# Kernel optimization log

Hardware: AMD Instinct MI355X
Metric: run time of the kernel (lower is better)

The kernel has to match this reference:

```python
import jax, jax.numpy as jnp
import numpy as np

DIM = 1024
RANK = 16


def setup_inputs() -> dict:
    key = jax.random.key(0)
    ks = jax.random.split(key, 9)
    s = 0.02
    return {
        "x": jax.random.normal(ks[0], (2, 4096, DIM), dtype=jnp.float32),
        "W_qkv": jax.random.normal(ks[1], (3 * DIM, DIM), dtype=jnp.float32) * s,
        "b_qkv": jax.random.normal(ks[2], (3 * DIM,), dtype=jnp.float32) * s,
        "A_q": jax.random.normal(ks[3], (RANK, DIM), dtype=jnp.float32) * s,
        "B_q": jax.random.normal(ks[4], (DIM, RANK), dtype=jnp.float32) * s,
        "A_k": jax.random.normal(ks[5], (RANK, DIM), dtype=jnp.float32) * s,
        "B_k": jax.random.normal(ks[6], (DIM, RANK), dtype=jnp.float32) * s,
        "A_v": jax.random.normal(ks[7], (RANK, DIM), dtype=jnp.float32) * s,
        "B_v": jax.random.normal(ks[8], (DIM, RANK), dtype=jnp.float32) * s,
        "alpha": jnp.float32(0.5),
    }


def reference(x, W_qkv, b_qkv, A_q, B_q, A_k, B_k, A_v, B_v, alpha):
    # base fused QKV projection: [B, S, 3*dim]
    qkv = jnp.einsum("bsd,od->bso", x, W_qkv) + b_qkv
    # low-rank adapters: x @ A.T @ B.T, rank=16
    lora_q = jnp.einsum("bsr,dr->bsd", jnp.einsum("bsd,rd->bsr", x, A_q), B_q)
    lora_k = jnp.einsum("bsr,dr->bsd", jnp.einsum("bsd,rd->bsr", x, A_k), B_k)
    lora_v = jnp.einsum("bsr,dr->bsd", jnp.einsum("bsd,rd->bsr", x, A_v), B_v)
    # scaled add into q/k/v slices (concat order matches torch slice layout)
    delta = jnp.concatenate([lora_q, lora_k, lora_v], axis=-1)
    return qkv + alpha * delta
```

## Files before the change

### kernel.cpp

```cpp
#include <hip/hip_runtime.h>
#include <stdint.h>

#define DIM    1024
#define RANK   16
#define M_TOT  8192
#define N_TOT  3072
#define K_TOT  1024

#define BM 128
#define BN 128
#define BK 64

typedef __attribute__((ext_vector_type(8))) short  s8v;
typedef __attribute__((ext_vector_type(4))) float  f4v;

__device__ __forceinline__ unsigned short f2bf(float f) {
    union { float f; unsigned int u; } v; v.f = f;
    unsigned int u = v.u;
    u += 0x7FFFu + ((u >> 16) & 1u);
    return (unsigned short)(u >> 16);
}

__global__ void cvt_x(const float4* __restrict__ x, ushort4* __restrict__ xb, int n4) {
    int i = blockIdx.x * blockDim.x + threadIdx.x;
    if (i < n4) {
        float4 v = x[i];
        ushort4 o;
        o.x = f2bf(v.x); o.y = f2bf(v.y); o.z = f2bf(v.z); o.w = f2bf(v.w);
        xb[i] = o;
    }
}

__global__ void fold_w(const float* __restrict__ W,
                       const float* __restrict__ Aq, const float* __restrict__ Bq,
                       const float* __restrict__ Ak, const float* __restrict__ Bk,
                       const float* __restrict__ Av, const float* __restrict__ Bv,
                       const float* __restrict__ alpha_p,
                       unsigned short* __restrict__ Wb) {
    const int o   = blockIdx.x;
    const int tid = threadIdx.x;
    const int sel  = o >> 10;
    const int orow = o & 1023;
    const float* Am = (sel == 0) ? Aq : (sel == 1) ? Ak : Av;
    const float* Bm = (sel == 0) ? Bq : (sel == 1) ? Bk : Bv;

    __shared__ float sb[RANK];
    if (tid < RANK) sb[tid] = alpha_p[0] * Bm[orow * RANK + tid];
    __syncthreads();

    for (int d = tid; d < DIM; d += 256) {
        float acc = W[o * DIM + d];
        #pragma unroll
        for (int r = 0; r < RANK; ++r)
            acc += sb[r] * Am[r * DIM + d];
        Wb[o * DIM + d] = f2bf(acc);
    }
}

__global__ __launch_bounds__(256, 2)
void gemm_bt(const unsigned short* __restrict__ Xb,
             const unsigned short* __restrict__ Wb,
             const float* __restrict__ bias,
             float* __restrict__ out) {
    __shared__ __align__(16) unsigned short As[BM * BK];
    __shared__ __align__(16) unsigned short Bs[BN * BK];

    const int tid  = threadIdx.x;
    const int wave = tid >> 6;
    const int lane = tid & 63;
    const int l15  = lane & 15;
    const int lq   = lane >> 4;
    const int wr   = wave >> 1;
    const int wc   = wave & 1;

    const int bm = blockIdx.x;
    const int bn = blockIdx.y;

    const unsigned short* aptr[4];
    const unsigned short* bptr[4];
    #pragma unroll
    for (int u = 0; u < 4; ++u) {
        const int c   = wave * 4 + u;
        const int row = ((c >> 1) << 4) + l15;
        const int col = ((c & 1) << 5) + (lq << 3);
        aptr[u] = Xb + (size_t)(bm * BM + row) * K_TOT + col;
        bptr[u] = Wb + (size_t)(bn * BN + row) * K_TOT + col;
    }

    f4v acc[4][4] = {};

    for (int kk = 0; kk < K_TOT; kk += BK) {
        __syncthreads();
        #pragma unroll
        for (int u = 0; u < 4; ++u) {
            const int c = wave * 4 + u;
            __builtin_amdgcn_global_load_lds(
                (const __attribute__((address_space(1))) void*)(aptr[u]),
                (__attribute__((address_space(3))) void*)(&As[c * 512]),
                16, 0, 0);
            __builtin_amdgcn_global_load_lds(
                (const __attribute__((address_space(1))) void*)(bptr[u]),
                (__attribute__((address_space(3))) void*)(&Bs[c * 512]),
                16, 0, 0);
            aptr[u] += BK;
            bptr[u] += BK;
        }
        __syncthreads();

        const s8v* Av = (const s8v*)As;
        const s8v* Bv = (const s8v*)Bs;
        #pragma unroll
        for (int t = 0; t < 2; ++t) {
            s8v af[4], bf[4];
            #pragma unroll
            for (int i = 0; i < 4; ++i) {
                const int ia = wr * 4 + i;
                const int jb = wc * 4 + i;
                af[i] = Av[(ia * 2 + t) * 64 + lane];
                bf[i] = Bv[(jb * 2 + t) * 64 + lane];
            }
            #pragma unroll
            for (int i = 0; i < 4; ++i)
                #pragma unroll
                for (int j = 0; j < 4; ++j)
                    acc[i][j] = __builtin_amdgcn_mfma_f32_16x16x32_bf16(
                        af[i], bf[j], acc[i][j], 0, 0, 0);
        }
    }

    const int col_base = bn * BN + wc * 64;
    const int row_base = bm * BM + wr * 64 + lq * 4;
    #pragma unroll
    for (int j = 0; j < 4; ++j) {
        const int col = col_base + j * 16 + l15;
        const float bv = bias[col];
        #pragma unroll
        for (int i = 0; i < 4; ++i) {
            const int row = row_base + i * 16;
            #pragma unroll
            for (int r = 0; r < 4; ++r)
                out[(size_t)(row + r) * N_TOT + col] = acc[i][j][r] + bv;
        }
    }
}

extern "C" void kernel_launch(void* const* d_in, const int* in_sizes, int n_in,
                              void* d_out, int out_size, void* d_ws, size_t ws_size,
                              hipStream_t stream) {
    const float* x     = (const float*)d_in[0];
    const float* W     = (const float*)d_in[1];
    const float* b     = (const float*)d_in[2];
    const float* Aq    = (const float*)d_in[3];
    const float* Bq    = (const float*)d_in[4];
    const float* Ak    = (const float*)d_in[5];
    const float* Bk    = (const float*)d_in[6];
    const float* Av    = (const float*)d_in[7];
    const float* Bv    = (const float*)d_in[8];
    const float* alpha = (const float*)d_in[9];
    float* out = (float*)d_out;

    unsigned short* xb = (unsigned short*)d_ws;
    unsigned short* Wb = (unsigned short*)((char*)d_ws + (size_t)M_TOT * K_TOT * 2);

    const int n4 = (M_TOT * K_TOT) / 4;
    cvt_x<<<n4 / 256, 256, 0, stream>>>((const float4*)x, (ushort4*)xb, n4);
    fold_w<<<N_TOT, 256, 0, stream>>>(W, Aq, Bq, Ak, Bk, Av, Bv, alpha, Wb);

    dim3 grid(M_TOT / BM, N_TOT / BN);
    gemm_bt<<<grid, 256, 0, stream>>>(xb, Wb, b, out);
}
```

Baseline: 249.9 us.

## Merge prep kernels and shrink GEMM M-tile to 64 for higher occupancy

Folds the x-to-bf16 conversion and the LoRA weight folding into one prep launch, removing a kernel launch gap. The GEMM block tile drops from 128x128 to 64x128. Each wave now computes a 64x32 strip with a 4x2 accumulator array, and launch bounds are raised to 5 blocks per CU. This doubles the grid and raises occupancy to hide latency, at the cost of less data reuse per block and more global traffic for the W tile.

Result: slower. 286.8 us (+14.8%).

```diff
diff --git a/kernel.cpp b/kernel.cpp
--- a/kernel.cpp
+++ b/kernel.cpp
@@ -7,7 +7,7 @@
 #define N_TOT  3072
 #define K_TOT  1024
 
-#define BM 128
+#define BM 64
 #define BN 128
 #define BK 64
 
@@ -21,43 +21,42 @@
     return (unsigned short)(u >> 16);
 }
 
-__global__ void cvt_x(const float4* __restrict__ x, ushort4* __restrict__ xb, int n4) {
-    int i = blockIdx.x * blockDim.x + threadIdx.x;
-    if (i < n4) {
+__global__ void prep(const float4* __restrict__ x, ushort4* __restrict__ xb,
+                     const float* __restrict__ W,
+                     const float* __restrict__ Aq, const float* __restrict__ Bq,
+                     const float* __restrict__ Ak, const float* __restrict__ Bk,
+                     const float* __restrict__ Av, const float* __restrict__ Bv,
+                     const float* __restrict__ alpha_p,
+                     unsigned short* __restrict__ Wb) {
+    const int tid = threadIdx.x;
+    if (blockIdx.x < 8192) {
+        int i = blockIdx.x * 256 + tid;
         float4 v = x[i];
         ushort4 o;
         o.x = f2bf(v.x); o.y = f2bf(v.y); o.z = f2bf(v.z); o.w = f2bf(v.w);
         xb[i] = o;
+    } else {
+        const int o    = blockIdx.x - 8192;
+        const int sel  = o >> 10;
+        const int orow = o & 1023;
+        const float* Am = (sel == 0) ? Aq : (sel == 1) ? Ak : Av;
+        const float* Bm = (sel == 0) ? Bq : (sel == 1) ? Bk : Bv;
+
+        __shared__ float sb[RANK];
+        if (tid < RANK) sb[tid] = alpha_p[0] * Bm[orow * RANK + tid];
+        __syncthreads();
+
+        for (int d = tid; d < DIM; d += 256) {
+            float acc = W[o * DIM + d];
+            #pragma unroll
+            for (int r = 0; r < RANK; ++r)
+                acc += sb[r] * Am[r * DIM + d];
+            Wb[o * DIM + d] = f2bf(acc);
+        }
     }
 }
 
-__global__ void fold_w(const float* __restrict__ W,
-                       const float* __restrict__ Aq, const float* __restrict__ Bq,
-                       const float* __restrict__ Ak, const float* __restrict__ Bk,
-                       const float* __restrict__ Av, const float* __restrict__ Bv,
-                       const float* __restrict__ alpha_p,
-                       unsigned short* __restrict__ Wb) {
-    const int o   = blockIdx.x;
-    const int tid = threadIdx.x;
-    const int sel  = o >> 10;
-    const int orow = o & 1023;
-    const float* Am = (sel == 0) ? Aq : (sel == 1) ? Ak : Av;
-    const float* Bm = (sel == 0) ? Bq : (sel == 1) ? Bk : Bv;
-
-    __shared__ float sb[RANK];
-    if (tid < RANK) sb[tid] = alpha_p[0] * Bm[orow * RANK + tid];
-    __syncthreads();
-
-    for (int d = tid; d < DIM; d += 256) {
-        float acc = W[o * DIM + d];
-        #pragma unroll
-        for (int r = 0; r < RANK; ++r)
-            acc += sb[r] * Am[r * DIM + d];
-        Wb[o * DIM + d] = f2bf(acc);
-    }
-}
-
-__global__ __launch_bounds__(256, 2)
+__global__ __launch_bounds__(256, 5)
 void gemm_bt(const unsigned short* __restrict__ Xb,
              const unsigned short* __restrict__ Wb,
              const float* __restrict__ bias,
@@ -70,76 +69,71 @@
     const int lane = tid & 63;
     const int l15  = lane & 15;
     const int lq   = lane >> 4;
-    const int wr   = wave >> 1;
-    const int wc   = wave & 1;
 
     const int bm = blockIdx.x;
     const int bn = blockIdx.y;
 
-    const unsigned short* aptr[4];
-    const unsigned short* bptr[4];
+    const unsigned short* gptr[6];
+    unsigned short* lptr[6];
     #pragma unroll
-    for (int u = 0; u < 4; ++u) {
-        const int c   = wave * 4 + u;
+    for (int u = 0; u < 6; ++u) {
+        const int q = wave * 6 + u;
+        const int c   = (q < 8) ? q : (q - 8);
         const int row = ((c >> 1) << 4) + l15;
         const int col = ((c & 1) << 5) + (lq << 3);
-        aptr[u] = Xb + (size_t)(bm * BM + row) * K_TOT + col;
-        bptr[u] = Wb + (size_t)(bn * BN + row) * K_TOT + col;
+        if (q < 8) {
+            gptr[u] = Xb + (size_t)(bm * BM + row) * K_TOT + col;
+            lptr[u] = &As[c * 512];
+        } else {
+            gptr[u] = Wb + (size_t)(bn * BN + row) * K_TOT + col;
+            lptr[u] = &Bs[c * 512];
+        }
     }
 
-    f4v acc[4][4] = {};
+    f4v acc[4][2] = {};
 
     for (int kk = 0; kk < K_TOT; kk += BK) {
         __syncthreads();
         #pragma unroll
-        for (int u = 0; u < 4; ++u) {
-            const int c = wave * 4 + u;
+        for (int u = 0; u < 6; ++u) {
             __builtin_amdgcn_global_load_lds(
-                (const __attribute__((address_space(1))) void*)(aptr[u]),
-                (__attribute__((address_space(3))) void*)(&As[c * 512]),
+                (const __attribute__((address_space(1))) void*)(gptr[u]),
+                (__attribute__((address_space(3))) void*)(lptr[u]),
                 16, 0, 0);
-            __builtin_amdgcn_global_load_lds(
-                (const __attribute__((address_space(1))) void*)(bptr[u]),
-                (__attribute__((address_space(3))) void*)(&Bs[c * 512]),
-                16, 0, 0);
-            aptr[u] += BK;
-            bptr[u] += BK;
+            gptr[u] += BK;
         }
         __syncthreads();
 
-        const s8v* Av = (const s8v*)As;
-        const s8v* Bv = (const s8v*)Bs;
+        const s8v* Avp = (const s8v*)As;
+        const s8v* Bvp = (const s8v*)Bs;
         #pragma unroll
         for (int t = 0; t < 2; ++t) {
-            s8v af[4], bf[4];
+            s8v af[4], bf[2];
             #pragma unroll
-            for (int i = 0; i < 4; ++i) {
-                const int ia = wr * 4 + i;
-                const int jb = wc * 4 + i;
-                af[i] = Av[(ia * 2 + t) * 64 + lane];
-                bf[i] = Bv[(jb * 2 + t) * 64 + lane];
-            }
+            for (int i = 0; i < 4; ++i)
+                af[i] = Avp[(i * 2 + t) * 64 + lane];
+            #pragma unroll
+            for (int j = 0; j < 2; ++j)
+                bf[j] = Bvp[((wave * 2 + j) * 2 + t) * 64 + lane];
             #pragma unroll
             for (int i = 0; i < 4; ++i)
                 #pragma unroll
-                for (int j = 0; j < 4; ++j)
+                for (int j = 0; j < 2; ++j)
                     acc[i][j] = __builtin_amdgcn_mfma_f32_16x16x32_bf16(
                         af[i], bf[j], acc[i][j], 0, 0, 0);
         }
     }
 
-    const int col_base = bn * BN + wc * 64;
-    const int row_base = bm * BM + wr * 64 + lq * 4;
     #pragma unroll
-    for (int j = 0; j < 4; ++j) {
-        const int col = col_base + j * 16 + l15;
+    for (int j = 0; j < 2; ++j) {
+        const int col = bn * BN + wave * 32 + j * 16 + l15;
         const float bv = bias[col];
         #pragma unroll
         for (int i = 0; i < 4; ++i) {
-            const int row = row_base + i * 16;
+            const int row0 = bm * BM + i * 16 + lq * 4;
             #pragma unroll
             for (int r = 0; r < 4; ++r)
-                out[(size_t)(row + r) * N_TOT + col] = acc[i][j][r] + bv;
+                out[(size_t)(row0 + r) * N_TOT + col] = acc[i][j][r] + bv;
         }
     }
 }
@@ -162,9 +156,8 @@
     unsigned short* xb = (unsigned short*)d_ws;
     unsigned short* Wb = (unsigned short*)((char*)d_ws + (size_t)M_TOT * K_TOT * 2);
 
-    const int n4 = (M_TOT * K_TOT) / 4;
-    cvt_x<<<n4 / 256, 256, 0, stream>>>((const float4*)x, (ushort4*)xb, n4);
-    fold_w<<<N_TOT, 256, 0, stream>>>(W, Aq, Bq, Ak, Bk, Av, Bv, alpha, Wb);
+    prep<<<8192 + N_TOT, 256, 0, stream>>>((const float4*)x, (ushort4*)xb,
+                                           W, Aq, Bq, Ak, Bk, Av, Bv, alpha, Wb);
 
     dim3 grid(M_TOT / BM, N_TOT / BN);
     gemm_bt<<<grid, 256, 0, stream>>>(xb, Wb, b, out);
```

## Merge prep kernels and register-prefetch next K tile in GEMM

Applied to the files above, without the earlier changes.

Merges the x conversion and the weight-folding kernels into a single launch that picks its work by block index, removing one launch and letting the two run concurrently. In the GEMM, the direct global-to-LDS loads are replaced by register prefetch: the next K tile is read into registers while MFMAs run on the current LDS tile, then written to LDS at the top of the next iteration. The launch bound is raised to 3 blocks per CU to target higher occupancy. The register staging uses more VGPRs and adds explicit LDS stores, and the last iteration issues a redundant prefetch that wraps back to offset 0.

Measured after the change: 244.5 us. -2.2%, faster.

```diff
diff --git a/kernel.cpp b/kernel.cpp
--- a/kernel.cpp
+++ b/kernel.cpp
@@ -21,43 +21,42 @@
     return (unsigned short)(u >> 16);
 }
 
-__global__ void cvt_x(const float4* __restrict__ x, ushort4* __restrict__ xb, int n4) {
-    int i = blockIdx.x * blockDim.x + threadIdx.x;
-    if (i < n4) {
+__global__ void prep(const float4* __restrict__ x, ushort4* __restrict__ xb,
+                     const float* __restrict__ W,
+                     const float* __restrict__ Aq, const float* __restrict__ Bq,
+                     const float* __restrict__ Ak, const float* __restrict__ Bk,
+                     const float* __restrict__ Av, const float* __restrict__ Bv,
+                     const float* __restrict__ alpha_p,
+                     unsigned short* __restrict__ Wb) {
+    const int tid = threadIdx.x;
+    if (blockIdx.x < 8192) {
+        int i = blockIdx.x * 256 + tid;
         float4 v = x[i];
         ushort4 o;
         o.x = f2bf(v.x); o.y = f2bf(v.y); o.z = f2bf(v.z); o.w = f2bf(v.w);
         xb[i] = o;
+    } else {
+        const int o    = blockIdx.x - 8192;
+        const int sel  = o >> 10;
+        const int orow = o & 1023;
+        const float* Am = (sel == 0) ? Aq : (sel == 1) ? Ak : Av;
+        const float* Bm = (sel == 0) ? Bq : (sel == 1) ? Bk : Bv;
+
+        __shared__ float sb[RANK];
+        if (tid < RANK) sb[tid] = alpha_p[0] * Bm[orow * RANK + tid];
+        __syncthreads();
+
+        for (int d = tid; d < DIM; d += 256) {
+            float acc = W[o * DIM + d];
+            #pragma unroll
+            for (int r = 0; r < RANK; ++r)
+                acc += sb[r] * Am[r * DIM + d];
+            Wb[o * DIM + d] = f2bf(acc);
+        }
     }
 }
 
-__global__ void fold_w(const float* __restrict__ W,
-                       const float* __restrict__ Aq, const float* __restrict__ Bq,
-                       const float* __restrict__ Ak, const float* __restrict__ Bk,
-                       const float* __restrict__ Av, const float* __restrict__ Bv,
-                       const float* __restrict__ alpha_p,
-                       unsigned short* __restrict__ Wb) {
-    const int o   = blockIdx.x;
-    const int tid = threadIdx.x;
-    const int sel  = o >> 10;
-    const int orow = o & 1023;
-    const float* Am = (sel == 0) ? Aq : (sel == 1) ? Ak : Av;
-    const float* Bm = (sel == 0) ? Bq : (sel == 1) ? Bk : Bv;
-
-    __shared__ float sb[RANK];
-    if (tid < RANK) sb[tid] = alpha_p[0] * Bm[orow * RANK + tid];
-    __syncthreads();
-
-    for (int d = tid; d < DIM; d += 256) {
-        float acc = W[o * DIM + d];
-        #pragma unroll
-        for (int r = 0; r < RANK; ++r)
-            acc += sb[r] * Am[r * DIM + d];
-        Wb[o * DIM + d] = f2bf(acc);
-    }
-}
-
-__global__ __launch_bounds__(256, 2)
+__global__ __launch_bounds__(256, 3)
 void gemm_bt(const unsigned short* __restrict__ Xb,
              const unsigned short* __restrict__ Wb,
              const float* __restrict__ bias,
@@ -78,6 +77,8 @@
 
     const unsigned short* aptr[4];
     const unsigned short* bptr[4];
+    unsigned short* alds[4];
+    unsigned short* blds[4];
     #pragma unroll
     for (int u = 0; u < 4; ++u) {
         const int c   = wave * 4 + u;
@@ -85,6 +86,15 @@
         const int col = ((c & 1) << 5) + (lq << 3);
         aptr[u] = Xb + (size_t)(bm * BM + row) * K_TOT + col;
         bptr[u] = Wb + (size_t)(bn * BN + row) * K_TOT + col;
+        alds[u] = &As[c * 512 + lane * 8];
+        blds[u] = &Bs[c * 512 + lane * 8];
+    }
+
+    s8v areg[4], breg[4];
+    #pragma unroll
+    for (int u = 0; u < 4; ++u) {
+        areg[u] = *(const s8v*)(aptr[u]);
+        breg[u] = *(const s8v*)(bptr[u]);
     }
 
     f4v acc[4][4] = {};
@@ -93,22 +103,20 @@
         __syncthreads();
         #pragma unroll
         for (int u = 0; u < 4; ++u) {
-            const int c = wave * 4 + u;
-            __builtin_amdgcn_global_load_lds(
-                (const __attribute__((address_space(1))) void*)(aptr[u]),
-                (__attribute__((address_space(3))) void*)(&As[c * 512]),
-                16, 0, 0);
-            __builtin_amdgcn_global_load_lds(
-                (const __attribute__((address_space(1))) void*)(bptr[u]),
-                (__attribute__((address_space(3))) void*)(&Bs[c * 512]),
-                16, 0, 0);
-            aptr[u] += BK;
-            bptr[u] += BK;
+            *(s8v*)(alds[u]) = areg[u];
+            *(s8v*)(blds[u]) = breg[u];
         }
         __syncthreads();
 
-        const s8v* Av = (const s8v*)As;
-        const s8v* Bv = (const s8v*)Bs;
+        const int kn = (kk + BK < K_TOT) ? (kk + BK) : 0;
+        #pragma unroll
+        for (int u = 0; u < 4; ++u) {
+            areg[u] = *(const s8v*)(aptr[u] + kn);
+            breg[u] = *(const s8v*)(bptr[u] + kn);
+        }
+
+        const s8v* Avp = (const s8v*)As;
+        const s8v* Bvp = (const s8v*)Bs;
         #pragma unroll
         for (int t = 0; t < 2; ++t) {
             s8v af[4], bf[4];
@@ -116,8 +124,8 @@
             for (int i = 0; i < 4; ++i) {
                 const int ia = wr * 4 + i;
                 const int jb = wc * 4 + i;
-                af[i] = Av[(ia * 2 + t) * 64 + lane];
-                bf[i] = Bv[(jb * 2 + t) * 64 + lane];
+                af[i] = Avp[(ia * 2 + t) * 64 + lane];
+                bf[i] = Bvp[(jb * 2 + t) * 64 + lane];
             }
             #pragma unroll
             for (int i = 0; i < 4; ++i)
@@ -162,9 +170,8 @@
     unsigned short* xb = (unsigned short*)d_ws;
     unsigned short* Wb = (unsigned short*)((char*)d_ws + (size_t)M_TOT * K_TOT * 2);
 
-    const int n4 = (M_TOT * K_TOT) / 4;
-    cvt_x<<<n4 / 256, 256, 0, stream>>>((const float4*)x, (ushort4*)xb, n4);
-    fold_w<<<N_TOT, 256, 0, stream>>>(W, Aq, Bq, Ak, Bk, Av, Bv, alpha, Wb);
+    prep<<<8192 + N_TOT, 256, 0, stream>>>((const float4*)x, (ushort4*)xb,
+                                           W, Aq, Bq, Ak, Bk, Av, Bv, alpha, Wb);
 
     dim3 grid(M_TOT / BM, N_TOT / BN);
     gemm_bt<<<grid, 256, 0, stream>>>(xb, Wb, b, out);
```
